# Kernel tuning notes

Hardware: AMD Instinct MI355X
Metric: run time of the kernel (lower is better)

Reference implementation:

```python
import jax, jax.numpy as jnp
import numpy as np
from jax import lax

DN = ('NCHW', 'OIHW', 'NCHW')


def _bilinear(img, py, px):
    # img: [B,C,H,W]; py,px: [B,K2,H,W] float sampling coords (zero outside)
    B, C, H, W = img.shape
    y0 = jnp.floor(py); x0 = jnp.floor(px)
    wy1 = py - y0; wy0 = 1.0 - wy1
    wx1 = px - x0; wx0 = 1.0 - wx1

    def gather(yi, xi):
        yc = jnp.clip(yi, 0, H - 1).astype(jnp.int32)
        xc = jnp.clip(xi, 0, W - 1).astype(jnp.int32)
        valid = ((yi >= 0) & (yi <= H - 1) & (xi >= 0) & (xi <= W - 1)).astype(img.dtype)
        # per-batch advanced gather -> [B,C,K2,H,W]
        g = jax.vmap(lambda im, a, b: im[:, a, b])(img, yc, xc)
        return g * valid[:, None]

    return (gather(y0, x0) * (wy0 * wx0)[:, None]
            + gather(y0, x0 + 1) * (wy0 * wx1)[:, None]
            + gather(y0 + 1, x0) * (wy1 * wx0)[:, None]
            + gather(y0 + 1, x0 + 1) * (wy1 * wx1)[:, None])


def _deform_layer(x, ow, ob, w, b, dil=1):
    # offset conv: 3x3, stride 1, pad 1 -> [B, 18, H, W]
    B, C, H, W = x.shape
    off = lax.conv_general_dilated(x, ow, (1, 1), 'SAME', dimension_numbers=DN)
    off = off + ob[None, :, None, None]
    off = off.reshape(B, 9, 2, H, W)  # per kernel point: (dy, dx)
    oy, ox = off[:, :, 0], off[:, :, 1]
    ky, kx = jnp.meshgrid(jnp.arange(3), jnp.arange(3), indexing='ij')
    ky = ky.reshape(9).astype(x.dtype); kx = kx.reshape(9).astype(x.dtype)
    yy = jnp.arange(H, dtype=x.dtype)[:, None]
    xx = jnp.arange(W, dtype=x.dtype)[None, :]
    # sampling coords: out_pos - pad + dil*k + offset (pad == dil)
    py = yy[None, None] - dil + dil * ky[None, :, None, None] + oy
    px = xx[None, None] - dil + dil * kx[None, :, None, None] + ox
    sam = _bilinear(x, py, px)  # [B,C,9,H,W]
    out = jnp.einsum('bckhw,ock->bohw', sam, w.reshape(w.shape[0], C, 9))
    return out + b[None, :, None, None]


def setup_inputs() -> dict:
    key = jax.random.key(0)
    ks = jax.random.split(key, 5)
    L, C = 4, 256
    x = jax.random.normal(ks[0], (2, C, 96, 96), dtype=jnp.float32)
    # small offset-conv weights -> moderate offsets (torch inits them to 0)
    off_w = jax.random.normal(ks[1], (L, 18, C, 3, 3), dtype=jnp.float32) * 0.01
    off_b = jnp.zeros((L, 18), dtype=jnp.float32)
    fan_in = C * 9
    dw = jax.random.normal(ks[2], (L, C, C, 3, 3), dtype=jnp.float32) * np.sqrt(2.0 / fan_in)
    db = jnp.zeros((L, C), dtype=jnp.float32)
    return {'x': x, 'off_w': off_w, 'off_b': off_b, 'dw': dw, 'db': db}


def reference(x, off_w, off_b, dw, db):
    L = off_w.shape[0]
    for i in range(L):
        x = _deform_layer(x, off_w[i], off_b[i], dw[i], db[i], dil=1)
        x = jax.nn.relu(x)
    return x
```

## Files before the change

### kernel.cpp

```cpp
#include <hip/hip_runtime.h>
#include <hip/hip_bf16.h>

#define BN 2
#define CH 256
#define HH 96
#define WW 96
#define NL 4
#define HW (HH*WW)
#define KK (CH*9)
#define NPOS (BN*HW)

#define MPOS 32
#define NBLK (NPOS/MPOS)
#define CKCH 32
#define CKLEN (CKCH*9)
#define NCKS 4
#define SAMW2 296

#define WB_PER_L (288*256*8)
#define WB_TOT (NL*WB_PER_L)
#define OWB_PER_L (288*32*8)
#define OWB_TOT (NL*OWB_PER_L)

typedef __attribute__((ext_vector_type(8))) short short8;
typedef __attribute__((ext_vector_type(4))) float f32x4;

__device__ __forceinline__ unsigned short f2bf(float f) {
    union { float f; unsigned int u; } v; v.f = f;
    unsigned int r = v.u + 0x7fffu + ((v.u >> 16) & 1u);
    return (unsigned short)(r >> 16);
}
__device__ __forceinline__ unsigned int pack_bf2(float lo, float hi) {
    float2 t; t.x = lo; t.y = hi;
    __hip_bfloat162 hb = __float22bfloat162_rn(t);
    unsigned int u; __builtin_memcpy(&u, &hb, 4);
    return u;
}

__global__ void prep_kernel(const float* __restrict__ dw, const float* __restrict__ off_w,
                            unsigned short* __restrict__ wB, unsigned short* __restrict__ owB,
                            unsigned short* __restrict__ xT) {
    int idx = blockIdx.x * 256 + threadIdx.x;
    if (idx < WB_TOT) {
        int j  = idx & 7;
        int oc = (idx >> 3) & 255;
        int g  = (idx >> 11) % 288;
        int l  = idx / WB_PER_L;
        int col = g * 8 + j;
        int ck = col / CKLEN;
        int r  = col - ck * CKLEN;
        int t9 = r >> 5;
        int ci = r & 31;
        int c  = ck * CKCH + ci;
        wB[idx] = f2bf(dw[((size_t)(l * CH + oc) * CH + c) * 9 + t9]);
    } else if (idx < WB_TOT + OWB_TOT) {
        int i2 = idx - WB_TOT;
        int j   = i2 & 7;
        int ocp = (i2 >> 3) & 31;
        int g   = (i2 >> 8) % 288;
        int l   = i2 / OWB_PER_L;
        int col = g * 8 + j;
        int ck = col / CKLEN;
        int r  = col - ck * CKLEN;
        int t9 = r >> 5;
        int ci = r & 31;
        int c  = ck * CKCH + ci;
        owB[i2] = (ocp < 18) ? f2bf(off_w[((size_t)(l * 18 + ocp) * CH + c) * 9 + t9]) : 0;
    } else if (idx < WB_TOT + OWB_TOT + CH) {
        xT[(size_t)NPOS * CH + (idx - WB_TOT - OWB_TOT)] = 0;
    }
}

__global__ void __launch_bounds__(256)
transpose_kernel(const float* __restrict__ src, unsigned short* __restrict__ xT) {
    __shared__ float tile[64][65];
    int blk = blockIdx.x;
    int b = blk / 576, r = blk - 576 * b;
    int hw0 = (r >> 2) * 64, c0 = (r & 3) * 64;
    int tid = threadIdx.x;
    int lane = tid & 63, grp = tid >> 6;
    const float* sp = src + (size_t)(b * CH + c0) * HW + hw0;
    #pragma unroll
    for (int i = 0; i < 16; ++i) {
        int c = grp * 16 + i;
        tile[c][lane] = sp[(size_t)c * HW + lane];
    }
    __syncthreads();
    unsigned short* dp = xT + (size_t)(b * HW + hw0) * CH + c0;
    #pragma unroll
    for (int i = 0; i < 16; ++i) {
        int hw = grp * 16 + i;
        dp[(size_t)hw * CH + lane] = f2bf(tile[lane][hw]);
    }
}

__global__ void __launch_bounds__(256)
off_mfma_kernel(const unsigned short* __restrict__ xT, const unsigned short* __restrict__ owB,
                float* __restrict__ off_p) {
    __shared__ int rtab[MPOS * 9];
    const int tid = threadIdx.x;
    const int sp  = (int)blockIdx.x & 3;
    int pb = (int)blockIdx.x >> 2;
    pb = (pb & 7) * (NBLK / 8) + (pb >> 3);
    const int pos0 = pb * MPOS;
    const int b0   = pos0 / HW;
    const int rem0 = pos0 - b0 * HW;
    const int h0   = rem0 / WW;
    const int w0   = rem0 - h0 * WW;
    const int zrel = (NPOS - b0 * HW) * CH;

    for (int rec = tid; rec < MPOS * 9; rec += 256) {
        int p = rec / 9, t9 = rec - 9 * p;
        int dy = t9 / 3 - 1, dx = t9 - 3 * (t9 / 3) - 1;
        int y = h0 + dy, xw = w0 + p + dx;
        bool valid = ((unsigned)y < HH) && ((unsigned)xw < WW);
        rtab[rec] = valid ? (y * WW + xw) * CH : zrel;
    }
    __syncthreads();

    const int m   = tid & 15;
    const int q   = (tid >> 4) & 3;
    const int wvi = tid >> 6;
    const int mt  = wvi & 1;
    const int nt  = wvi >> 1;
    const int p   = mt * 16 + m;

    int s0[9];
    #pragma unroll
    for (int kb = 0; kb < 9; ++kb) s0[kb] = rtab[p * 9 + kb];

    const unsigned short* xq = xT + (size_t)b0 * HW * CH + q * 8 + (size_t)sp * 2 * CKCH;
    const unsigned short* wq = owB + (size_t)(nt * 16 + m) * 8
                                   + (size_t)(sp * 2 * 36 + q) * (32 * 8);

    f32x4 acc0 = {}, acc1 = {};
    #pragma unroll
    for (int kb = 0; kb < 9; ++kb) {
        short8 av0 = *(const short8*)(xq + s0[kb]);
        short8 av1 = *(const short8*)(xq + s0[kb] + CKCH);
        short8 bv0 = *(const short8*)(wq + (size_t)(kb * 4) * (32 * 8));
        short8 bv1 = *(const short8*)(wq + (size_t)(36 + kb * 4) * (32 * 8));
        acc0 = __builtin_amdgcn_mfma_f32_16x16x32_bf16(av0, bv0, acc0, 0, 0, 0);
        acc1 = __builtin_amdgcn_mfma_f32_16x16x32_bf16(av1, bv1, acc1, 0, 0, 0);
    }
    int oc = nt * 16 + m;
    if (oc < 18) {
        float* op = off_p + (size_t)sp * NPOS * 20 + oc;
        #pragma unroll
        for (int r = 0; r < 4; ++r) {
            int pp = mt * 16 + q * 4 + r;
            op[(size_t)(pos0 + pp) * 20] = acc0[r] + acc1[r];
        }
    }
}

__global__ void __launch_bounds__(256, 5)
deform_mfma_kernel(const unsigned short* __restrict__ xT, const float* __restrict__ off_p,
                   const float* __restrict__ ob, const unsigned short* __restrict__ wB,
                   float* __restrict__ dst0, float* __restrict__ dst1) {
    __shared__ __align__(16) unsigned short sam[MPOS * SAMW2];
    __shared__ float offs[MPOS * 18];
    __shared__ __align__(16) uint4 taps4[MPOS * 9];
    __shared__ unsigned short dso16[MPOS * 9];
    const int tid = threadIdx.x;
    const int s   = (int)blockIdx.x & 1;
    int pb = (int)blockIdx.x >> 1;
    pb = (pb & 7) * (NBLK / 8) + (pb >> 3);
    const int pos0 = pb * MPOS;
    const int b0   = pos0 / HW;
    const int rem0 = pos0 - b0 * HW;
    const int h0   = rem0 / WW;
    const int w0   = rem0 - h0 * WW;

    for (int i = tid; i < MPOS * 18; i += 256) {
        int p = i / 18, oc = i - 18 * p;
        const float* bp = off_p + (size_t)(pos0 + p) * 20 + oc;
        offs[i] = bp[0] + bp[(size_t)NPOS * 20] + bp[(size_t)NPOS * 40]
                + bp[(size_t)NPOS * 60] + ob[oc];
    }
    __syncthreads();

    for (int rec = tid; rec < MPOS * 9; rec += 256) {
        int p  = rec / 9, t9 = rec - 9 * p;
        int ky = t9 / 3, kx = t9 - 3 * (t9 / 3);
        float py = (float)(h0 - 1 + ky) + offs[p * 18 + 2 * t9];
        float px = (float)(w0 + p - 1 + kx) + offs[p * 18 + 2 * t9 + 1];
        float yf = floorf(py), xf = floorf(px);
        int y0 = (int)yf, x0 = (int)xf;
        float wy1 = py - yf, wx1 = px - xf;
        float fy0 = ((unsigned)y0       < HH) ? 1.f - wy1 : 0.f;
        float fy1 = ((unsigned)(y0 + 1) < HH) ? wy1       : 0.f;
        float fx0 = ((unsigned)x0       < WW) ? 1.f - wx1 : 0.f;
        float fx1 = ((unsigned)(x0 + 1) < WW) ? wx1       : 0.f;
        int y0c = min(max(y0, 0), HH - 1), y1c = min(max(y0 + 1, 0), HH - 1);
        int x0c = min(max(x0, 0), WW - 1), x1c = min(max(x0 + 1, 0), WW - 1);
        int bx  = min(max(x0, 0), WW - 2);
        float wA  = (x0c == bx     ? fx0 : 0.f) + (x1c == bx     ? fx1 : 0.f);
        float wBv = (x0c == bx + 1 ? fx0 : 0.f) + (x1c == bx + 1 ? fx1 : 0.f);
        uint4 tv;
        tv.x = (unsigned int)((y0c * WW + bx) * CH);
        tv.y = (unsigned int)((y1c * WW + bx) * CH);
        tv.z = pack_bf2(fy0 * wA, fy0 * wBv);
        tv.w = pack_bf2(fy1 * wA, fy1 * wBv);
        taps4[rec] = tv;
        dso16[rec] = (unsigned short)(p * SAMW2 + t9 * 32);
    }

    const int lane = tid & 63;
    const int wvi  = tid >> 6;
    const int cp   = lane & 15;
    const int rsub = lane >> 4;
    const int m    = tid & 15;
    const int q    = (tid >> 4) & 3;

    f32x4 acc[2][4] = {};
    const unsigned short* xTb = xT + (size_t)b0 * HW * CH;

    for (int ckl = 0; ckl < NCKS; ++ckl) {
        const int ck = s * NCKS + ckl;
        __syncthreads();
        const unsigned short* xs = xTb + ck * CKCH + cp * 2;
        #pragma unroll 3
        for (int rr = 0; rr < 18; ++rr) {
            int rec = wvi * 72 + rr * 4 + rsub;
            uint4 tv = taps4[rec];
            int dso  = dso16[rec];
            float u0 = __uint_as_float(tv.z << 16);
            float u1 = __uint_as_float(tv.z & 0xFFFF0000u);
            float u2 = __uint_as_float(tv.w << 16);
            float u3 = __uint_as_float(tv.w & 0xFFFF0000u);
            unsigned int A0, A1, C0, C1;
            __builtin_memcpy(&A0, xs + tv.x, 4);
            __builtin_memcpy(&A1, xs + tv.x + CH, 4);
            __builtin_memcpy(&C0, xs + tv.y, 4);
            __builtin_memcpy(&C1, xs + tv.y + CH, 4);
            float2 a0 = make_float2(__uint_as_float(A0 << 16), __uint_as_float(A0 & 0xFFFF0000u));
            float2 a1 = make_float2(__uint_as_float(A1 << 16), __uint_as_float(A1 & 0xFFFF0000u));
            float2 c0 = make_float2(__uint_as_float(C0 << 16), __uint_as_float(C0 & 0xFFFF0000u));
            float2 c1 = make_float2(__uint_as_float(C1 << 16), __uint_as_float(C1 & 0xFFFF0000u));
            float2 vv;
            vv.x = a0.x * u0;               vv.y = a0.y * u0;
            vv.x = fmaf(a1.x, u1, vv.x);    vv.y = fmaf(a1.y, u1, vv.y);
            vv.x = fmaf(c0.x, u2, vv.x);    vv.y = fmaf(c0.y, u2, vv.y);
            vv.x = fmaf(c1.x, u3, vv.x);    vv.y = fmaf(c1.y, u3, vv.y);
            *(unsigned int*)(sam + dso + cp * 2) = pack_bf2(vv.x, vv.y);
        }
        __syncthreads();
        const unsigned short* arow0 = sam + m * SAMW2 + q * 8;
        const unsigned short* arow1 = arow0 + 16 * SAMW2;
        const int g0 = ck * 36;
        for (int kb = 0; kb < 9; ++kb) {
            short8 av0 = *(const short8*)(arow0 + kb * 32);
            short8 av1 = *(const short8*)(arow1 + kb * 32);
            const unsigned short* wkb = wB + ((size_t)(g0 + kb * 4 + q) * 256
                                             + (wvi * 64 + m)) * 8;
            #pragma unroll
            for (int t = 0; t < 4; ++t) {
                short8 bv = *(const short8*)(wkb + t * 16 * 8);
                acc[0][t] = __builtin_amdgcn_mfma_f32_16x16x32_bf16(av0, bv, acc[0][t], 0, 0, 0);
                acc[1][t] = __builtin_amdgcn_mfma_f32_16x16x32_bf16(av1, bv, acc[1][t], 0, 0, 0);
            }
        }
    }

    float* dst = s ? dst1 : dst0;
    float* cT = (float*)sam;
    #pragma unroll
    for (int mt = 0; mt < 2; ++mt) {
        __syncthreads();
        #pragma unroll
        for (int t = 0; t < 4; ++t) {
            int oc = wvi * 64 + t * 16 + m;
            #pragma unroll
            for (int r = 0; r < 4; ++r)
                cT[oc * 17 + q * 4 + r] = acc[mt][t][r];
        }
        __syncthreads();
        float* dp = dst + (size_t)(pos0 + mt * 16) * CH + tid;
        #pragma unroll 4
        for (int p = 0; p < 16; ++p)
            dp[(size_t)p * CH] = cT[tid * 17 + p];
    }
}

__global__ void __launch_bounds__(256)
sum_cl_kernel(const float* __restrict__ p0, const float* __restrict__ p1,
              const float* __restrict__ db, unsigned short* __restrict__ xT) {
    unsigned int idx = blockIdx.x * 256 + threadIdx.x;
    unsigned int e = idx * 4;
    unsigned int oc = e & (CH - 1);
    float4 bsv = *(const float4*)(db + oc);
    float4 a = *(const float4*)(p0 + e);
    float4 b = *(const float4*)(p1 + e);
    unsigned int o2[2];
    o2[0] = pack_bf2(fmaxf(a.x + b.x + bsv.x, 0.f), fmaxf(a.y + b.y + bsv.y, 0.f));
    o2[1] = pack_bf2(fmaxf(a.z + b.z + bsv.z, 0.f), fmaxf(a.w + b.w + bsv.w, 0.f));
    __builtin_memcpy(xT + e, o2, 8);
}

__global__ void __launch_bounds__(256)
sum_nchw_kernel(const float* __restrict__ p0, const float* __restrict__ p1,
                const float* __restrict__ db, float* __restrict__ out) {
    __shared__ float tile[64][65];
    int blk = blockIdx.x;
    int hw0 = (blk >> 2) * 64;
    int oc0 = (blk & 3) * 64;
    int tid = threadIdx.x;
    int lane = tid & 63, grp = tid >> 6;
    float bsv = db[oc0 + lane];
    #pragma unroll
    for (int i = 0; i < 16; ++i) {
        int r = grp * 16 + i;
        size_t e = (size_t)(hw0 + r) * CH + oc0 + lane;
        tile[r][lane] = fmaxf(p0[e] + p1[e] + bsv, 0.f);
    }
    __syncthreads();
    int b = hw0 / HW, hwl = hw0 - b * HW;
    #pragma unroll
    for (int i = 0; i < 16; ++i) {
        int oc = grp * 16 + i;
        out[((size_t)(b * CH) + oc0 + oc) * HW + hwl + lane] = tile[lane][oc];
    }
}

extern "C" void kernel_launch(void* const* d_in, const int* in_sizes, int n_in,
                              void* d_out, int out_size, void* d_ws, size_t ws_size,
                              hipStream_t stream) {
    const float* x     = (const float*)d_in[0];
    const float* off_w = (const float*)d_in[1];
    const float* off_b = (const float*)d_in[2];
    const float* dw    = (const float*)d_in[3];
    const float* db    = (const float*)d_in[4];

    float* ws   = (float*)d_ws;
    float* p0    = ws;
    float* p1    = p0 + (size_t)NPOS * CH;
    float* off_p = p1 + (size_t)NPOS * CH;
    unsigned short* wB  = (unsigned short*)(off_p + (size_t)4 * NPOS * 20);
    unsigned short* owB = wB + WB_TOT;
    unsigned short* xT  = owB + OWB_TOT;

    prep_kernel<<<(WB_TOT + OWB_TOT + CH + 255) / 256, 256, 0, stream>>>(
        dw, off_w, wB, owB, xT);
    transpose_kernel<<<BN * 576, 256, 0, stream>>>(x, xT);

    for (int l = 0; l < NL; ++l) {
        off_mfma_kernel<<<NBLK * 4, 256, 0, stream>>>(
            xT, owB + (size_t)l * OWB_PER_L, off_p);
        deform_mfma_kernel<<<NBLK * 2, 256, 0, stream>>>(
            xT, off_p, off_b + l * 18, wB + (size_t)l * WB_PER_L, p0, p1);
        if (l < NL - 1)
            sum_cl_kernel<<<(NPOS * CH / 4) / 256, 256, 0, stream>>>(p0, p1, db + l * CH, xT);
        else
            sum_nchw_kernel<<<(NPOS / 64) * 4, 256, 0, stream>>>(p0, p1, db + l * CH,
                                                                 (float*)d_out);
    }
}
```

Measured before the change: 411.4 us.

## Double-buffer deform sample tile and split offset conv across eight K partials

```diff
diff --git a/kernel.cpp b/kernel.cpp
--- a/kernel.cpp
+++ b/kernel.cpp
@@ -16,6 +16,7 @@
 #define CKLEN (CKCH*9)
 #define NCKS 4
 #define SAMW2 296
+#define SAMSZ (MPOS*SAMW2)
 
 #define WB_PER_L (288*256*8)
 #define WB_TOT (NL*WB_PER_L)
@@ -122,43 +123,40 @@
     const int q   = (tid >> 4) & 3;
     const int wvi = tid >> 6;
     const int mt  = wvi & 1;
-    const int nt  = wvi >> 1;
+    const int kh  = wvi >> 1;
+    const int ck  = sp * 2 + kh;
     const int p   = mt * 16 + m;
 
     int s0[9];
     #pragma unroll
     for (int kb = 0; kb < 9; ++kb) s0[kb] = rtab[p * 9 + kb];
 
-    const unsigned short* xq = xT + (size_t)b0 * HW * CH + q * 8 + (size_t)sp * 2 * CKCH;
-    const unsigned short* wq = owB + (size_t)(nt * 16 + m) * 8
-                                   + (size_t)(sp * 2 * 36 + q) * (32 * 8);
+    const unsigned short* xq = xT + (size_t)b0 * HW * CH + q * 8 + (size_t)ck * CKCH;
+    const unsigned short* wq = owB + (size_t)(ck * 36 + q) * (32 * 8);
 
     f32x4 acc0 = {}, acc1 = {};
     #pragma unroll
     for (int kb = 0; kb < 9; ++kb) {
-        short8 av0 = *(const short8*)(xq + s0[kb]);
-        short8 av1 = *(const short8*)(xq + s0[kb] + CKCH);
-        short8 bv0 = *(const short8*)(wq + (size_t)(kb * 4) * (32 * 8));
-        short8 bv1 = *(const short8*)(wq + (size_t)(36 + kb * 4) * (32 * 8));
-        acc0 = __builtin_amdgcn_mfma_f32_16x16x32_bf16(av0, bv0, acc0, 0, 0, 0);
-        acc1 = __builtin_amdgcn_mfma_f32_16x16x32_bf16(av1, bv1, acc1, 0, 0, 0);
-    }
-    int oc = nt * 16 + m;
-    if (oc < 18) {
-        float* op = off_p + (size_t)sp * NPOS * 20 + oc;
-        #pragma unroll
-        for (int r = 0; r < 4; ++r) {
-            int pp = mt * 16 + q * 4 + r;
-            op[(size_t)(pos0 + pp) * 20] = acc0[r] + acc1[r];
-        }
-    }
-}
-
-__global__ void __launch_bounds__(256, 5)
+        short8 av  = *(const short8*)(xq + s0[kb]);
+        short8 bv0 = *(const short8*)(wq + (size_t)(kb * 4) * (32 * 8) + m * 8);
+        short8 bv1 = *(const short8*)(wq + (size_t)(kb * 4) * (32 * 8) + (16 + m) * 8);
+        acc0 = __builtin_amdgcn_mfma_f32_16x16x32_bf16(av, bv0, acc0, 0, 0, 0);
+        acc1 = __builtin_amdgcn_mfma_f32_16x16x32_bf16(av, bv1, acc1, 0, 0, 0);
+    }
+    float* op = off_p + (size_t)ck * NPOS * 20;
+    #pragma unroll
+    for (int r = 0; r < 4; ++r) {
+        int pp = pos0 + mt * 16 + q * 4 + r;
+        op[(size_t)pp * 20 + m] = acc0[r];
+        if (m < 2) op[(size_t)pp * 20 + 16 + m] = acc1[r];
+    }
+}
+
+__global__ void __launch_bounds__(256)
 deform_mfma_kernel(const unsigned short* __restrict__ xT, const float* __restrict__ off_p,
                    const float* __restrict__ ob, const unsigned short* __restrict__ wB,
                    float* __restrict__ dst0, float* __restrict__ dst1) {
-    __shared__ __align__(16) unsigned short sam[MPOS * SAMW2];
+    __shared__ __align__(16) unsigned short sam[2 * SAMSZ];
     __shared__ float offs[MPOS * 18];
     __shared__ __align__(16) uint4 taps4[MPOS * 9];
     __shared__ unsigned short dso16[MPOS * 9];
@@ -175,8 +173,10 @@
     for (int i = tid; i < MPOS * 18; i += 256) {
         int p = i / 18, oc = i - 18 * p;
         const float* bp = off_p + (size_t)(pos0 + p) * 20 + oc;
-        offs[i] = bp[0] + bp[(size_t)NPOS * 20] + bp[(size_t)NPOS * 40]
-                + bp[(size_t)NPOS * 60] + ob[oc];
+        float ssum = ob[oc];
+        #pragma unroll
+        for (int v = 0; v < 8; ++v) ssum += bp[(size_t)v * NPOS * 20];
+        offs[i] = ssum;
     }
     __syncthreads();
 
@@ -215,10 +215,12 @@
 
     f32x4 acc[2][4] = {};
     const unsigned short* xTb = xT + (size_t)b0 * HW * CH;
+    const unsigned short* arow0b = sam + m * SAMW2 + q * 8;
+    const unsigned short* arow1b = arow0b + 16 * SAMW2;
 
     for (int ckl = 0; ckl < NCKS; ++ckl) {
         const int ck = s * NCKS + ckl;
-        __syncthreads();
+        unsigned short* sw = sam + (ckl & 1) * SAMSZ;
         const unsigned short* xs = xTb + ck * CKCH + cp * 2;
         #pragma unroll 3
         for (int rr = 0; rr < 18; ++rr) {
@@ -243,12 +245,32 @@
             vv.x = fmaf(a1.x, u1, vv.x);    vv.y = fmaf(a1.y, u1, vv.y);
             vv.x = fmaf(c0.x, u2, vv.x);    vv.y = fmaf(c0.y, u2, vv.y);
             vv.x = fmaf(c1.x, u3, vv.x);    vv.y = fmaf(c1.y, u3, vv.y);
-            *(unsigned int*)(sam + dso + cp * 2) = pack_bf2(vv.x, vv.y);
+            *(unsigned int*)(sw + dso + cp * 2) = pack_bf2(vv.x, vv.y);
+        }
+        if (ckl > 0) {
+            const int pbuf = (ckl - 1) & 1;
+            const unsigned short* arow0 = arow0b + pbuf * SAMSZ;
+            const unsigned short* arow1 = arow1b + pbuf * SAMSZ;
+            const int g0 = (ck - 1) * 36;
+            for (int kb = 0; kb < 9; ++kb) {
+                short8 av0 = *(const short8*)(arow0 + kb * 32);
+                short8 av1 = *(const short8*)(arow1 + kb * 32);
+                const unsigned short* wkb = wB + ((size_t)(g0 + kb * 4 + q) * 256
+                                                 + (wvi * 64 + m)) * 8;
+                #pragma unroll
+                for (int t = 0; t < 4; ++t) {
+                    short8 bv = *(const short8*)(wkb + t * 16 * 8);
+                    acc[0][t] = __builtin_amdgcn_mfma_f32_16x16x32_bf16(av0, bv, acc[0][t], 0, 0, 0);
+                    acc[1][t] = __builtin_amdgcn_mfma_f32_16x16x32_bf16(av1, bv, acc[1][t], 0, 0, 0);
+                }
+            }
         }
         __syncthreads();
-        const unsigned short* arow0 = sam + m * SAMW2 + q * 8;
-        const unsigned short* arow1 = arow0 + 16 * SAMW2;
-        const int g0 = ck * 36;
+    }
+    {
+        const unsigned short* arow0 = arow0b + SAMSZ;
+        const unsigned short* arow1 = arow1b + SAMSZ;
+        const int g0 = (s * NCKS + NCKS - 1) * 36;
         for (int kb = 0; kb < 9; ++kb) {
             short8 av0 = *(const short8*)(arow0 + kb * 32);
             short8 av1 = *(const short8*)(arow1 + kb * 32);
@@ -336,7 +358,7 @@
     float* p0    = ws;
     float* p1    = p0 + (size_t)NPOS * CH;
     float* off_p = p1 + (size_t)NPOS * CH;
-    unsigned short* wB  = (unsigned short*)(off_p + (size_t)4 * NPOS * 20);
+    unsigned short* wB  = (unsigned short*)(off_p + (size_t)8 * NPOS * 20);
     unsigned short* owB = wB + WB_TOT;
     unsigned short* xT  = owB + OWB_TOT;
 
```

Result: slower. 472.3 us (+14.8%).
